# Kernel tuning notes

Hardware: AMD Instinct MI355X
Metric: run time of the kernel (lower is better)

The kernel has to match this reference:

```python
import jax, jax.numpy as jnp
import numpy as np

N = 8192
D_IN = 128
D_OUT = 64


def setup_inputs() -> dict:
    key = jax.random.key(0)
    k1, k2, k3 = jax.random.split(key, 3)
    features = jax.random.normal(k1, (N, D_IN), dtype=jnp.float32)
    # uniform [0,1) entries -> strictly positive row sums (degrees)
    adjacency_matrix = jax.random.uniform(k2, (N, N), dtype=jnp.float32)
    weight = jax.random.normal(k3, (D_IN, D_OUT), dtype=jnp.float32)
    return {"features": features, "adjacency_matrix": adjacency_matrix, "weight": weight}


def reference(features, adjacency_matrix, weight):
    # degree_matrix = diag(rowsum(A)); inverse(sqrt(diag(d))) == diag(d^{-1/2})
    deg = jnp.sum(adjacency_matrix, axis=1)            # [N]
    d_inv_sqrt = 1.0 / jnp.sqrt(deg)                   # [N]
    # D^{-1/2} A D^{-1/2} via broadcasting instead of dense diag matmuls
    norm_adj = d_inv_sqrt[:, None] * adjacency_matrix * d_inv_sqrt[None, :]  # [N,N]
    # (norm_adj @ X) @ W -- contract small dim last for efficiency
    h = norm_adj @ features                            # [N, D_IN]
    return jax.nn.relu(h @ weight)                     # [N, D_OUT]
```

## Files before the change

### kernel.cpp

```cpp
#include <hip/hip_runtime.h>

#define N_NODES 8192
#define D_IN    128
#define D_OUT   64
#define NSPLIT  16

typedef __attribute__((ext_vector_type(8))) short short8;
typedef __attribute__((ext_vector_type(4))) float f32x4;

__device__ __forceinline__ short f2bf(float f) {
    unsigned u = __builtin_bit_cast(unsigned, f);
    u += 0x7fff + ((u >> 16) & 1);
    return (short)(u >> 16);
}
__device__ __forceinline__ unsigned f2bf_pack(float lo, float hi) {
    unsigned a = __builtin_bit_cast(unsigned, lo);
    a += 0x7fff + ((a >> 16) & 1);
    unsigned b = __builtin_bit_cast(unsigned, hi);
    b += 0x7fff + ((b >> 16) & 1);
    return (a >> 16) | (b & 0xffff0000u);
}

__global__ __launch_bounds__(256) void k_deg(const float* __restrict__ A,
                                             float* __restrict__ dis,
                                             unsigned short* __restrict__ A16) {
    const int wave = threadIdx.x >> 6;
    const int lane = threadIdx.x & 63;
    const int row  = blockIdx.x * 4 + wave;
    const float4* Ar = (const float4*)(A + (size_t)row * N_NODES);
    uint2* Aw = (uint2*)(A16 + (size_t)row * N_NODES);
    float s = 0.f;
#pragma unroll
    for (int i = 0; i < 32; ++i) {
        float4 v = Ar[lane + 64 * i];
        s += (v.x + v.y) + (v.z + v.w);
        uint2 p;
        p.x = f2bf_pack(v.x, v.y);
        p.y = f2bf_pack(v.z, v.w);
        Aw[lane + 64 * i] = p;
    }
#pragma unroll
    for (int off = 32; off; off >>= 1) s += __shfl_down(s, off, 64);
    if (lane == 0) dis[row] = rsqrtf(s);
}

__global__ __launch_bounds__(256) void k_gpack(const float* __restrict__ X,
                                               const float* __restrict__ W,
                                               const float* __restrict__ dis,
                                               unsigned short* __restrict__ Gp) {
    __shared__ float Wl[D_IN * D_OUT];
    __shared__ float Xl[32 * 129];
    const int t = blockIdx.x, tid = threadIdx.x;

    const float4* W4 = (const float4*)W;
    float4* Wl4 = (float4*)Wl;
#pragma unroll
    for (int i = 0; i < 8; ++i) Wl4[tid + 256 * i] = W4[tid + 256 * i];
    const float4* X4 = (const float4*)(X + (size_t)t * 32 * D_IN);
#pragma unroll
    for (int i = 0; i < 4; ++i) {
        int idx = tid + 256 * i;
        float4 v = X4[idx];
        int r = idx >> 5, c = (idx & 31) * 4;
        float* dst = Xl + r * 129 + c;
        dst[0] = v.x; dst[1] = v.y; dst[2] = v.z; dst[3] = v.w;
    }
    __syncthreads();

    const int kl = tid & 31;
    const int nb = (tid >> 5) * 8;
    float acc[8] = {0.f,0.f,0.f,0.f,0.f,0.f,0.f,0.f};
    const float* xr = Xl + kl * 129;
    for (int d = 0; d < D_IN; ++d) {
        float xv = xr[d];
        const float* wr = Wl + d * D_OUT + nb;
#pragma unroll
        for (int c = 0; c < 8; ++c) acc[c] += xv * wr[c];
    }
    const float scale = dis[t * 32 + kl];
    const int quad = kl >> 3, j = kl & 7;
#pragma unroll
    for (int c = 0; c < 8; ++c) {
        int n = nb + c;
        int u = n >> 4;
        int lanei = quad * 16 + (n & 15);
        Gp[(((size_t)t * 4 + u) * 64 + lanei) * 8 + j] = (unsigned short)f2bf(acc[c] * scale);
    }
}

__global__ __launch_bounds__(256) void k_spmm(const unsigned short* __restrict__ A16,
                                              const unsigned short* __restrict__ Gp,
                                              float* __restrict__ partial) {
    const int lane = threadIdx.x & 63;
    const int wave = threadIdx.x >> 6;
    const int quad = lane >> 4;
    const int l15  = lane & 15;
    const int rowbase = blockIdx.x * 128 + wave * 32;

    const short8* Ar0 = (const short8*)(A16 + (size_t)(rowbase + l15) * N_NODES);
    const short8* Ar1 = (const short8*)(A16 + (size_t)(rowbase + 16 + l15) * N_NODES);
    const short8* Gq  = (const short8*)Gp;

    const int kt0 = blockIdx.y * (N_NODES / 32 / NSPLIT);
    f32x4 acc[2][4] = {};

    for (int kt = kt0; kt < kt0 + (N_NODES / 32 / NSPLIT); ++kt) {
        short8 a0 = Ar0[kt * 4 + quad];
        short8 a1 = Ar1[kt * 4 + quad];
        const short8* gb = Gq + (size_t)kt * 256 + lane;
#pragma unroll
        for (int u = 0; u < 4; ++u) {
            short8 b = gb[u * 64];
            acc[0][u] = __builtin_amdgcn_mfma_f32_16x16x32_bf16(a0, b, acc[0][u], 0, 0, 0);
            acc[1][u] = __builtin_amdgcn_mfma_f32_16x16x32_bf16(a1, b, acc[1][u], 0, 0, 0);
        }
    }

    float* P = partial + (size_t)blockIdx.y * (N_NODES * D_OUT);
#pragma unroll
    for (int rt = 0; rt < 2; ++rt)
#pragma unroll
        for (int u = 0; u < 4; ++u)
#pragma unroll
            for (int r = 0; r < 4; ++r) {
                int gr = rowbase + rt * 16 + quad * 4 + r;
                P[(size_t)gr * D_OUT + u * 16 + l15] = acc[rt][u][r];
            }
}

__global__ __launch_bounds__(256) void k_out(const float* __restrict__ partial,
                                             const float* __restrict__ dis,
                                             float* __restrict__ out) {
    const int idx = blockIdx.x * 256 + threadIdx.x;
    const float4* p4 = (const float4*)partial;
    float4 s = p4[idx];
#pragma unroll
    for (int sp = 1; sp < NSPLIT; ++sp) {
        float4 v = p4[idx + sp * (N_NODES * D_OUT / 4)];
        s.x += v.x; s.y += v.y; s.z += v.z; s.w += v.w;
    }
    const float sc = dis[idx >> 4];
    float4 o;
    o.x = fmaxf(s.x * sc, 0.f);
    o.y = fmaxf(s.y * sc, 0.f);
    o.z = fmaxf(s.z * sc, 0.f);
    o.w = fmaxf(s.w * sc, 0.f);
    ((float4*)out)[idx] = o;
}

extern "C" void kernel_launch(void* const* d_in, const int* in_sizes, int n_in,
                              void* d_out, int out_size, void* d_ws, size_t ws_size,
                              hipStream_t stream) {
    const float* X = (const float*)d_in[0];
    const float* A = (const float*)d_in[1];
    const float* W = (const float*)d_in[2];
    float* out = (float*)d_out;

    char* ws = (char*)d_ws;
    float*          dis     = (float*)ws;
    unsigned short* Gp      = (unsigned short*)(ws + (1u << 20));
    unsigned short* A16     = (unsigned short*)(ws + (2u << 20));
    float*          partial = (float*)(ws + (2u << 20) + ((size_t)128 << 20));

    k_deg  <<<N_NODES / 4, 256, 0, stream>>>(A, dis, A16);
    k_gpack<<<N_NODES / 32, 256, 0, stream>>>(X, W, dis, Gp);
    k_spmm <<<dim3(N_NODES / 128, NSPLIT), 256, 0, stream>>>(A16, Gp, partial);
    k_out  <<<(N_NODES * D_OUT / 4) / 256, 256, 0, stream>>>(partial, dis, out);
}
```

Before: 434.1 us.

## Fuse four kernels into one cooperative persistent kernel with grid syncs

Replaces the four separate launches (degree/convert, G pack, MFMA SpMM, split reduce) with one cooperative persistent kernel whose phases are separated by grid.sync, sized from occupancy and capped at 1024 blocks. The split-K factor is halved, which shrinks the partial buffer and the reduction work but leaves fewer parallel SpMM work items. The G-pack phase drops its LDS staging and reads W and X straight from global memory. This is meant to remove launch gaps and tail effects, at the cost of grid-sync overhead and possibly lower occupancy; if the cooperative launch fails, four kernels with fixed grids run instead.

```diff
diff --git a/kernel.cpp b/kernel.cpp
--- a/kernel.cpp
+++ b/kernel.cpp
@@ -1,9 +1,13 @@
 #include <hip/hip_runtime.h>
+#include <hip/hip_cooperative_groups.h>
+
+namespace cg = cooperative_groups;
 
 #define N_NODES 8192
 #define D_IN    128
 #define D_OUT   64
-#define NSPLIT  16
+#define NSPLIT  8
+#define MAXGRID 1024
 
 typedef __attribute__((ext_vector_type(8))) short short8;
 typedef __attribute__((ext_vector_type(4))) float f32x4;
@@ -21,131 +25,162 @@
     return (a >> 16) | (b & 0xffff0000u);
 }
 
-__global__ __launch_bounds__(256) void k_deg(const float* __restrict__ A,
-                                             float* __restrict__ dis,
-                                             unsigned short* __restrict__ A16) {
-    const int wave = threadIdx.x >> 6;
-    const int lane = threadIdx.x & 63;
-    const int row  = blockIdx.x * 4 + wave;
-    const float4* Ar = (const float4*)(A + (size_t)row * N_NODES);
-    uint2* Aw = (uint2*)(A16 + (size_t)row * N_NODES);
-    float s = 0.f;
-#pragma unroll
-    for (int i = 0; i < 32; ++i) {
-        float4 v = Ar[lane + 64 * i];
-        s += (v.x + v.y) + (v.z + v.w);
-        uint2 p;
-        p.x = f2bf_pack(v.x, v.y);
-        p.y = f2bf_pack(v.z, v.w);
-        Aw[lane + 64 * i] = p;
-    }
-#pragma unroll
-    for (int off = 32; off; off >>= 1) s += __shfl_down(s, off, 64);
-    if (lane == 0) dis[row] = rsqrtf(s);
-}
-
-__global__ __launch_bounds__(256) void k_gpack(const float* __restrict__ X,
-                                               const float* __restrict__ W,
-                                               const float* __restrict__ dis,
-                                               unsigned short* __restrict__ Gp) {
-    __shared__ float Wl[D_IN * D_OUT];
-    __shared__ float Xl[32 * 129];
-    const int t = blockIdx.x, tid = threadIdx.x;
-
-    const float4* W4 = (const float4*)W;
-    float4* Wl4 = (float4*)Wl;
-#pragma unroll
-    for (int i = 0; i < 8; ++i) Wl4[tid + 256 * i] = W4[tid + 256 * i];
-    const float4* X4 = (const float4*)(X + (size_t)t * 32 * D_IN);
-#pragma unroll
-    for (int i = 0; i < 4; ++i) {
-        int idx = tid + 256 * i;
-        float4 v = X4[idx];
-        int r = idx >> 5, c = (idx & 31) * 4;
-        float* dst = Xl + r * 129 + c;
-        dst[0] = v.x; dst[1] = v.y; dst[2] = v.z; dst[3] = v.w;
-    }
-    __syncthreads();
-
-    const int kl = tid & 31;
-    const int nb = (tid >> 5) * 8;
-    float acc[8] = {0.f,0.f,0.f,0.f,0.f,0.f,0.f,0.f};
-    const float* xr = Xl + kl * 129;
-    for (int d = 0; d < D_IN; ++d) {
-        float xv = xr[d];
-        const float* wr = Wl + d * D_OUT + nb;
-#pragma unroll
-        for (int c = 0; c < 8; ++c) acc[c] += xv * wr[c];
-    }
-    const float scale = dis[t * 32 + kl];
-    const int quad = kl >> 3, j = kl & 7;
-#pragma unroll
-    for (int c = 0; c < 8; ++c) {
-        int n = nb + c;
-        int u = n >> 4;
-        int lanei = quad * 16 + (n & 15);
-        Gp[(((size_t)t * 4 + u) * 64 + lanei) * 8 + j] = (unsigned short)f2bf(acc[c] * scale);
-    }
-}
-
-__global__ __launch_bounds__(256) void k_spmm(const unsigned short* __restrict__ A16,
-                                              const unsigned short* __restrict__ Gp,
-                                              float* __restrict__ partial) {
-    const int lane = threadIdx.x & 63;
-    const int wave = threadIdx.x >> 6;
-    const int quad = lane >> 4;
-    const int l15  = lane & 15;
-    const int rowbase = blockIdx.x * 128 + wave * 32;
-
-    const short8* Ar0 = (const short8*)(A16 + (size_t)(rowbase + l15) * N_NODES);
-    const short8* Ar1 = (const short8*)(A16 + (size_t)(rowbase + 16 + l15) * N_NODES);
-    const short8* Gq  = (const short8*)Gp;
-
-    const int kt0 = blockIdx.y * (N_NODES / 32 / NSPLIT);
-    f32x4 acc[2][4] = {};
-
-    for (int kt = kt0; kt < kt0 + (N_NODES / 32 / NSPLIT); ++kt) {
-        short8 a0 = Ar0[kt * 4 + quad];
-        short8 a1 = Ar1[kt * 4 + quad];
-        const short8* gb = Gq + (size_t)kt * 256 + lane;
-#pragma unroll
-        for (int u = 0; u < 4; ++u) {
-            short8 b = gb[u * 64];
-            acc[0][u] = __builtin_amdgcn_mfma_f32_16x16x32_bf16(a0, b, acc[0][u], 0, 0, 0);
-            acc[1][u] = __builtin_amdgcn_mfma_f32_16x16x32_bf16(a1, b, acc[1][u], 0, 0, 0);
-        }
-    }
-
-    float* P = partial + (size_t)blockIdx.y * (N_NODES * D_OUT);
-#pragma unroll
-    for (int rt = 0; rt < 2; ++rt)
-#pragma unroll
-        for (int u = 0; u < 4; ++u)
-#pragma unroll
-            for (int r = 0; r < 4; ++r) {
-                int gr = rowbase + rt * 16 + quad * 4 + r;
-                P[(size_t)gr * D_OUT + u * 16 + l15] = acc[rt][u][r];
+__device__ __forceinline__ void phase1(const float* __restrict__ A,
+                                       float* __restrict__ dis,
+                                       unsigned short* __restrict__ A16,
+                                       int bid, int nb, int tid) {
+    const int wave = tid >> 6, lane = tid & 63;
+    for (int row = bid * 4 + wave; row < N_NODES; row += nb * 4) {
+        const float4* Ar = (const float4*)(A + (size_t)row * N_NODES);
+        uint2* Aw = (uint2*)(A16 + (size_t)row * N_NODES);
+        float s = 0.f;
+#pragma unroll
+        for (int i = 0; i < 32; ++i) {
+            float4 v = Ar[lane + 64 * i];
+            s += (v.x + v.y) + (v.z + v.w);
+            uint2 p;
+            p.x = f2bf_pack(v.x, v.y);
+            p.y = f2bf_pack(v.z, v.w);
+            Aw[lane + 64 * i] = p;
+        }
+#pragma unroll
+        for (int off = 32; off; off >>= 1) s += __shfl_down(s, off, 64);
+        if (lane == 0) dis[row] = rsqrtf(s);
+    }
+}
+
+__device__ __forceinline__ void phase2(const float* __restrict__ X,
+                                       const float* __restrict__ W,
+                                       const float* __restrict__ dis,
+                                       unsigned short* __restrict__ Gp,
+                                       int bid, int nb, int tid) {
+    for (int gid = bid * 256 + tid; gid < N_NODES * 8; gid += nb * 256) {
+        const int k = gid >> 3;
+        const int n0 = (gid & 7) * 8;
+        float acc[8] = {0.f,0.f,0.f,0.f,0.f,0.f,0.f,0.f};
+        const float4* Xr = (const float4*)(X + (size_t)k * D_IN);
+#pragma unroll 4
+        for (int d4 = 0; d4 < 32; ++d4) {
+            float4 xv = Xr[d4];
+            const float* w = W + (d4 * 4) * D_OUT + n0;
+#pragma unroll
+            for (int q = 0; q < 4; ++q) {
+                float x = (q == 0) ? xv.x : (q == 1) ? xv.y : (q == 2) ? xv.z : xv.w;
+                float4 w0 = ((const float4*)(w + q * D_OUT))[0];
+                float4 w1 = ((const float4*)(w + q * D_OUT))[1];
+                acc[0] += x * w0.x; acc[1] += x * w0.y;
+                acc[2] += x * w0.z; acc[3] += x * w0.w;
+                acc[4] += x * w1.x; acc[5] += x * w1.y;
+                acc[6] += x * w1.z; acc[7] += x * w1.w;
             }
-}
-
-__global__ __launch_bounds__(256) void k_out(const float* __restrict__ partial,
-                                             const float* __restrict__ dis,
-                                             float* __restrict__ out) {
-    const int idx = blockIdx.x * 256 + threadIdx.x;
-    const float4* p4 = (const float4*)partial;
-    float4 s = p4[idx];
-#pragma unroll
-    for (int sp = 1; sp < NSPLIT; ++sp) {
-        float4 v = p4[idx + sp * (N_NODES * D_OUT / 4)];
-        s.x += v.x; s.y += v.y; s.z += v.z; s.w += v.w;
-    }
-    const float sc = dis[idx >> 4];
-    float4 o;
-    o.x = fmaxf(s.x * sc, 0.f);
-    o.y = fmaxf(s.y * sc, 0.f);
-    o.z = fmaxf(s.z * sc, 0.f);
-    o.w = fmaxf(s.w * sc, 0.f);
-    ((float4*)out)[idx] = o;
+        }
+        const float scale = dis[k];
+        const int t = k >> 5, quad = (k >> 3) & 3, j = k & 7;
+#pragma unroll
+        for (int c = 0; c < 8; ++c) {
+            int n = n0 + c;
+            Gp[(((size_t)t * 4 + (n >> 4)) * 64 + quad * 16 + (n & 15)) * 8 + j] =
+                (unsigned short)f2bf(acc[c] * scale);
+        }
+    }
+}
+
+__device__ __forceinline__ void phase3(const unsigned short* __restrict__ A16,
+                                       const unsigned short* __restrict__ Gp,
+                                       float* __restrict__ partial,
+                                       int bid, int nb, int tid) {
+    const int wave = tid >> 6, lane = tid & 63;
+    const int quad = lane >> 4, l15 = lane & 15;
+    const short8* Gq = (const short8*)Gp;
+    for (int w = bid; w < 64 * NSPLIT; w += nb) {
+        const int rowbase = (w & 63) * 128 + wave * 32;
+        const int split = w >> 6;
+        const short8* Ar0 = (const short8*)(A16 + (size_t)(rowbase + l15) * N_NODES);
+        const short8* Ar1 = (const short8*)(A16 + (size_t)(rowbase + 16 + l15) * N_NODES);
+        const int kt0 = split * (N_NODES / 32 / NSPLIT);
+        f32x4 acc[2][4] = {};
+        for (int kt = kt0; kt < kt0 + (N_NODES / 32 / NSPLIT); ++kt) {
+            short8 a0 = Ar0[kt * 4 + quad];
+            short8 a1 = Ar1[kt * 4 + quad];
+            const short8* gb = Gq + (size_t)kt * 256 + lane;
+#pragma unroll
+            for (int u = 0; u < 4; ++u) {
+                short8 b = gb[u * 64];
+                acc[0][u] = __builtin_amdgcn_mfma_f32_16x16x32_bf16(a0, b, acc[0][u], 0, 0, 0);
+                acc[1][u] = __builtin_amdgcn_mfma_f32_16x16x32_bf16(a1, b, acc[1][u], 0, 0, 0);
+            }
+        }
+        float* P = partial + (size_t)split * (N_NODES * D_OUT);
+#pragma unroll
+        for (int rt = 0; rt < 2; ++rt)
+#pragma unroll
+            for (int u = 0; u < 4; ++u)
+#pragma unroll
+                for (int r = 0; r < 4; ++r)
+                    P[(size_t)(rowbase + rt * 16 + quad * 4 + r) * D_OUT + u * 16 + l15] =
+                        acc[rt][u][r];
+    }
+}
+
+__device__ __forceinline__ void phase4(const float* __restrict__ partial,
+                                       const float* __restrict__ dis,
+                                       float* __restrict__ out,
+                                       int bid, int nb, int tid) {
+    for (int gid = bid * 256 + tid; gid < N_NODES * D_OUT / 4; gid += nb * 256) {
+        const float4* p4 = (const float4*)partial;
+        float4 s = p4[gid];
+#pragma unroll
+        for (int sp = 1; sp < NSPLIT; ++sp) {
+            float4 v = p4[gid + sp * (N_NODES * D_OUT / 4)];
+            s.x += v.x; s.y += v.y; s.z += v.z; s.w += v.w;
+        }
+        const float sc = dis[gid >> 4];
+        float4 o;
+        o.x = fmaxf(s.x * sc, 0.f);
+        o.y = fmaxf(s.y * sc, 0.f);
+        o.z = fmaxf(s.z * sc, 0.f);
+        o.w = fmaxf(s.w * sc, 0.f);
+        ((float4*)out)[gid] = o;
+    }
+}
+
+__global__ __launch_bounds__(256, 2) void k_fused(
+    const float* __restrict__ A, const float* __restrict__ X,
+    const float* __restrict__ W, float* __restrict__ dis,
+    unsigned short* __restrict__ A16, unsigned short* __restrict__ Gp,
+    float* __restrict__ partial, float* __restrict__ out)
+{
+    cg::grid_group grid = cg::this_grid();
+    const int bid = blockIdx.x, nb = gridDim.x, tid = threadIdx.x;
+    phase1(A, dis, A16, bid, nb, tid);
+    grid.sync();
+    phase2(X, W, dis, Gp, bid, nb, tid);
+    grid.sync();
+    phase3(A16, Gp, partial, bid, nb, tid);
+    grid.sync();
+    phase4(partial, dis, out, bid, nb, tid);
+}
+
+__global__ __launch_bounds__(256) void k_p1(const float* __restrict__ A,
+                                            float* __restrict__ dis,
+                                            unsigned short* __restrict__ A16) {
+    phase1(A, dis, A16, blockIdx.x, gridDim.x, threadIdx.x);
+}
+__global__ __launch_bounds__(256) void k_p2(const float* __restrict__ X,
+                                            const float* __restrict__ W,
+                                            const float* __restrict__ dis,
+                                            unsigned short* __restrict__ Gp) {
+    phase2(X, W, dis, Gp, blockIdx.x, gridDim.x, threadIdx.x);
+}
+__global__ __launch_bounds__(256) void k_p3(const unsigned short* __restrict__ A16,
+                                            const unsigned short* __restrict__ Gp,
+                                            float* __restrict__ partial) {
+    phase3(A16, Gp, partial, blockIdx.x, gridDim.x, threadIdx.x);
+}
+__global__ __launch_bounds__(256) void k_p4(const float* __restrict__ partial,
+                                            const float* __restrict__ dis,
+                                            float* __restrict__ out) {
+    phase4(partial, dis, out, blockIdx.x, gridDim.x, threadIdx.x);
 }
 
 extern "C" void kernel_launch(void* const* d_in, const int* in_sizes, int n_in,
@@ -162,8 +197,21 @@
     unsigned short* A16     = (unsigned short*)(ws + (2u << 20));
     float*          partial = (float*)(ws + (2u << 20) + ((size_t)128 << 20));
 
-    k_deg  <<<N_NODES / 4, 256, 0, stream>>>(A, dis, A16);
-    k_gpack<<<N_NODES / 32, 256, 0, stream>>>(X, W, dis, Gp);
-    k_spmm <<<dim3(N_NODES / 128, NSPLIT), 256, 0, stream>>>(A16, Gp, partial);
-    k_out  <<<(N_NODES * D_OUT / 4) / 256, 256, 0, stream>>>(partial, dis, out);
-}
+    int perCU = 0;
+    if (hipOccupancyMaxActiveBlocksPerMultiprocessor(&perCU, (const void*)k_fused,
+                                                     256, 0) != hipSuccess || perCU < 1)
+        perCU = 1;
+    int nblk = perCU * 256;
+    if (nblk > MAXGRID) nblk = MAXGRID;
+
+    void* args[] = { (void*)&A, (void*)&X, (void*)&W, (void*)&dis,
+                     (void*)&A16, (void*)&Gp, (void*)&partial, (void*)&out };
+    hipError_t err = hipLaunchCooperativeKernel((const void*)k_fused, dim3(nblk),
+                                                dim3(256), args, 0, stream);
+    if (err != hipSuccess) {
+        k_p1<<<2048, 256, 0, stream>>>(A, dis, A16);
+        k_p2<<<256, 256, 0, stream>>>(X, W, dis, Gp);
+        k_p3<<<512, 256, 0, stream>>>(A16, Gp, partial);
+        k_p4<<<512, 256, 0, stream>>>(partial, dis, out);
+    }
+}
```

Measured after the change: 621.3 us. 43.1% more time.

## Convert A to bf16 inside the matmul kernel instead of staging a bf16 copy

Applied to the files above, without the earlier changes.

Removes the bf16 copy of the adjacency matrix written by the degree kernel; the matmul kernel now reads fp32 A directly and converts it to bf16 in registers before the MFMAs. This eliminates a 128MB write and changes the memory traffic mix, at the cost of reading twice as many bytes of A in the matmul and extra conversion ALU work. It also doubles the K-split count (adding partial-sum traffic), rewrites the X·W kernel without shared memory, and batches loads in the degree kernel.

```diff
diff --git a/kernel.cpp b/kernel.cpp
--- a/kernel.cpp
+++ b/kernel.cpp
@@ -3,7 +3,7 @@
 #define N_NODES 8192
 #define D_IN    128
 #define D_OUT   64
-#define NSPLIT  16
+#define NSPLIT  32
 
 typedef __attribute__((ext_vector_type(8))) short short8;
 typedef __attribute__((ext_vector_type(4))) float f32x4;
@@ -13,31 +13,20 @@
     u += 0x7fff + ((u >> 16) & 1);
     return (short)(u >> 16);
 }
-__device__ __forceinline__ unsigned f2bf_pack(float lo, float hi) {
-    unsigned a = __builtin_bit_cast(unsigned, lo);
-    a += 0x7fff + ((a >> 16) & 1);
-    unsigned b = __builtin_bit_cast(unsigned, hi);
-    b += 0x7fff + ((b >> 16) & 1);
-    return (a >> 16) | (b & 0xffff0000u);
-}
 
 __global__ __launch_bounds__(256) void k_deg(const float* __restrict__ A,
-                                             float* __restrict__ dis,
-                                             unsigned short* __restrict__ A16) {
-    const int wave = threadIdx.x >> 6;
-    const int lane = threadIdx.x & 63;
-    const int row  = blockIdx.x * 4 + wave;
+                                             float* __restrict__ dis) {
+    const int wave = threadIdx.x >> 6, lane = threadIdx.x & 63;
+    const int row = blockIdx.x * 4 + wave;
     const float4* Ar = (const float4*)(A + (size_t)row * N_NODES);
-    uint2* Aw = (uint2*)(A16 + (size_t)row * N_NODES);
     float s = 0.f;
 #pragma unroll
-    for (int i = 0; i < 32; ++i) {
-        float4 v = Ar[lane + 64 * i];
-        s += (v.x + v.y) + (v.z + v.w);
-        uint2 p;
-        p.x = f2bf_pack(v.x, v.y);
-        p.y = f2bf_pack(v.z, v.w);
-        Aw[lane + 64 * i] = p;
+    for (int i = 0; i < 4; ++i) {
+        float4 v[8];
+#pragma unroll
+        for (int j = 0; j < 8; ++j) v[j] = Ar[lane + 64 * (i * 8 + j)];
+#pragma unroll
+        for (int j = 0; j < 8; ++j) s += (v[j].x + v[j].y) + (v[j].z + v[j].w);
     }
 #pragma unroll
     for (int off = 32; off; off >>= 1) s += __shfl_down(s, off, 64);
@@ -48,104 +37,100 @@
                                                const float* __restrict__ W,
                                                const float* __restrict__ dis,
                                                unsigned short* __restrict__ Gp) {
-    __shared__ float Wl[D_IN * D_OUT];
-    __shared__ float Xl[32 * 129];
-    const int t = blockIdx.x, tid = threadIdx.x;
-
-    const float4* W4 = (const float4*)W;
-    float4* Wl4 = (float4*)Wl;
+    const int gid = blockIdx.x * 256 + threadIdx.x;
+    if (gid >= N_NODES * 8) return;
+    const int k = gid >> 3;
+    const int n0 = (gid & 7) * 8;
+    float acc[8] = {0.f,0.f,0.f,0.f,0.f,0.f,0.f,0.f};
+    const float4* Xr = (const float4*)(X + (size_t)k * D_IN);
+#pragma unroll 4
+    for (int d4 = 0; d4 < 32; ++d4) {
+        float4 xv = Xr[d4];
+        const float* w = W + (d4 * 4) * D_OUT + n0;
 #pragma unroll
-    for (int i = 0; i < 8; ++i) Wl4[tid + 256 * i] = W4[tid + 256 * i];
-    const float4* X4 = (const float4*)(X + (size_t)t * 32 * D_IN);
-#pragma unroll
-    for (int i = 0; i < 4; ++i) {
-        int idx = tid + 256 * i;
-        float4 v = X4[idx];
-        int r = idx >> 5, c = (idx & 31) * 4;
-        float* dst = Xl + r * 129 + c;
-        dst[0] = v.x; dst[1] = v.y; dst[2] = v.z; dst[3] = v.w;
+        for (int q = 0; q < 4; ++q) {
+            float x = (q == 0) ? xv.x : (q == 1) ? xv.y : (q == 2) ? xv.z : xv.w;
+            float4 w0 = ((const float4*)(w + q * D_OUT))[0];
+            float4 w1 = ((const float4*)(w + q * D_OUT))[1];
+            acc[0] += x * w0.x; acc[1] += x * w0.y;
+            acc[2] += x * w0.z; acc[3] += x * w0.w;
+            acc[4] += x * w1.x; acc[5] += x * w1.y;
+            acc[6] += x * w1.z; acc[7] += x * w1.w;
+        }
     }
-    __syncthreads();
-
-    const int kl = tid & 31;
-    const int nb = (tid >> 5) * 8;
-    float acc[8] = {0.f,0.f,0.f,0.f,0.f,0.f,0.f,0.f};
-    const float* xr = Xl + kl * 129;
-    for (int d = 0; d < D_IN; ++d) {
-        float xv = xr[d];
-        const float* wr = Wl + d * D_OUT + nb;
-#pragma unroll
-        for (int c = 0; c < 8; ++c) acc[c] += xv * wr[c];
-    }
-    const float scale = dis[t * 32 + kl];
-    const int quad = kl >> 3, j = kl & 7;
+    const float scale = dis[k];
+    const int t = k >> 5, quad = (k >> 3) & 3, j = k & 7;
 #pragma unroll
     for (int c = 0; c < 8; ++c) {
-        int n = nb + c;
-        int u = n >> 4;
-        int lanei = quad * 16 + (n & 15);
-        Gp[(((size_t)t * 4 + u) * 64 + lanei) * 8 + j] = (unsigned short)f2bf(acc[c] * scale);
+        int n = n0 + c;
+        Gp[(((size_t)t * 4 + (n >> 4)) * 64 + quad * 16 + (n & 15)) * 8 + j] =
+            (unsigned short)f2bf(acc[c] * scale);
     }
 }
 
-__global__ __launch_bounds__(256) void k_spmm(const unsigned short* __restrict__ A16,
-                                              const unsigned short* __restrict__ Gp,
-                                              float* __restrict__ partial) {
-    const int lane = threadIdx.x & 63;
-    const int wave = threadIdx.x >> 6;
-    const int quad = lane >> 4;
-    const int l15  = lane & 15;
+__global__ __launch_bounds__(256, 4) void k_spmm(const float* __restrict__ A,
+                                                 const unsigned short* __restrict__ Gp,
+                                                 float* __restrict__ partial) {
+    const int lane = threadIdx.x & 63, wave = threadIdx.x >> 6;
+    const int quad = lane >> 4, l15 = lane & 15;
     const int rowbase = blockIdx.x * 128 + wave * 32;
-
-    const short8* Ar0 = (const short8*)(A16 + (size_t)(rowbase + l15) * N_NODES);
-    const short8* Ar1 = (const short8*)(A16 + (size_t)(rowbase + 16 + l15) * N_NODES);
-    const short8* Gq  = (const short8*)Gp;
-
+    const float* Ar0 = A + (size_t)(rowbase + l15) * N_NODES;
+    const float* Ar1 = A + (size_t)(rowbase + 16 + l15) * N_NODES;
+    const short8* Gq = (const short8*)Gp;
     const int kt0 = blockIdx.y * (N_NODES / 32 / NSPLIT);
     f32x4 acc[2][4] = {};
-
+#pragma unroll 2
     for (int kt = kt0; kt < kt0 + (N_NODES / 32 / NSPLIT); ++kt) {
-        short8 a0 = Ar0[kt * 4 + quad];
-        short8 a1 = Ar1[kt * 4 + quad];
+        const int col = kt * 32 + quad * 8;
+        float4 a0lo = *(const float4*)(Ar0 + col);
+        float4 a0hi = *(const float4*)(Ar0 + col + 4);
+        float4 a1lo = *(const float4*)(Ar1 + col);
+        float4 a1hi = *(const float4*)(Ar1 + col + 4);
         const short8* gb = Gq + (size_t)kt * 256 + lane;
-#pragma unroll
-        for (int u = 0; u < 4; ++u) {
-            short8 b = gb[u * 64];
-            acc[0][u] = __builtin_amdgcn_mfma_f32_16x16x32_bf16(a0, b, acc[0][u], 0, 0, 0);
-            acc[1][u] = __builtin_amdgcn_mfma_f32_16x16x32_bf16(a1, b, acc[1][u], 0, 0, 0);
-        }
+        short8 b0 = gb[0], b1 = gb[64], b2 = gb[128], b3 = gb[192];
+        short8 a0, a1;
+        a0[0]=f2bf(a0lo.x); a0[1]=f2bf(a0lo.y); a0[2]=f2bf(a0lo.z); a0[3]=f2bf(a0lo.w);
+        a0[4]=f2bf(a0hi.x); a0[5]=f2bf(a0hi.y); a0[6]=f2bf(a0hi.z); a0[7]=f2bf(a0hi.w);
+        a1[0]=f2bf(a1lo.x); a1[1]=f2bf(a1lo.y); a1[2]=f2bf(a1lo.z); a1[3]=f2bf(a1lo.w);
+        a1[4]=f2bf(a1hi.x); a1[5]=f2bf(a1hi.y); a1[6]=f2bf(a1hi.z); a1[7]=f2bf(a1hi.w);
+        acc[0][0] = __builtin_amdgcn_mfma_f32_16x16x32_bf16(a0, b0, acc[0][0], 0, 0, 0);
+        acc[1][0] = __builtin_amdgcn_mfma_f32_16x16x32_bf16(a1, b0, acc[1][0], 0, 0, 0);
+        acc[0][1] = __builtin_amdgcn_mfma_f32_16x16x32_bf16(a0, b1, acc[0][1], 0, 0, 0);
+        acc[1][1] = __builtin_amdgcn_mfma_f32_16x16x32_bf16(a1, b1, acc[1][1], 0, 0, 0);
+        acc[0][2] = __builtin_amdgcn_mfma_f32_16x16x32_bf16(a0, b2, acc[0][2], 0, 0, 0);
+        acc[1][2] = __builtin_amdgcn_mfma_f32_16x16x32_bf16(a1, b2, acc[1][2], 0, 0, 0);
+        acc[0][3] = __builtin_amdgcn_mfma_f32_16x16x32_bf16(a0, b3, acc[0][3], 0, 0, 0);
+        acc[1][3] = __builtin_amdgcn_mfma_f32_16x16x32_bf16(a1, b3, acc[1][3], 0, 0, 0);
     }
-
     float* P = partial + (size_t)blockIdx.y * (N_NODES * D_OUT);
 #pragma unroll
     for (int rt = 0; rt < 2; ++rt)
 #pragma unroll
         for (int u = 0; u < 4; ++u)
 #pragma unroll
-            for (int r = 0; r < 4; ++r) {
-                int gr = rowbase + rt * 16 + quad * 4 + r;
-                P[(size_t)gr * D_OUT + u * 16 + l15] = acc[rt][u][r];
-            }
+            for (int r = 0; r < 4; ++r)
+                P[(size_t)(rowbase + rt * 16 + quad * 4 + r) * D_OUT + u * 16 + l15] =
+                    acc[rt][u][r];
 }
 
 __global__ __launch_bounds__(256) void k_out(const float* __restrict__ partial,
                                              const float* __restrict__ dis,
                                              float* __restrict__ out) {
-    const int idx = blockIdx.x * 256 + threadIdx.x;
+    const int gid = blockIdx.x * 256 + threadIdx.x;
     const float4* p4 = (const float4*)partial;
-    float4 s = p4[idx];
+    float4 s = p4[gid];
 #pragma unroll
     for (int sp = 1; sp < NSPLIT; ++sp) {
-        float4 v = p4[idx + sp * (N_NODES * D_OUT / 4)];
+        float4 v = p4[gid + (size_t)sp * (N_NODES * D_OUT / 4)];
         s.x += v.x; s.y += v.y; s.z += v.z; s.w += v.w;
     }
-    const float sc = dis[idx >> 4];
+    const float sc = dis[gid >> 4];
     float4 o;
     o.x = fmaxf(s.x * sc, 0.f);
     o.y = fmaxf(s.y * sc, 0.f);
     o.z = fmaxf(s.z * sc, 0.f);
     o.w = fmaxf(s.w * sc, 0.f);
-    ((float4*)out)[idx] = o;
+    ((float4*)out)[gid] = o;
 }
 
 extern "C" void kernel_launch(void* const* d_in, const int* in_sizes, int n_in,
@@ -159,11 +144,10 @@
     char* ws = (char*)d_ws;
     float*          dis     = (float*)ws;
     unsigned short* Gp      = (unsigned short*)(ws + (1u << 20));
-    unsigned short* A16     = (unsigned short*)(ws + (2u << 20));
-    float*          partial = (float*)(ws + (2u << 20) + ((size_t)128 << 20));
+    float*          partial = (float*)(ws + (4u << 20));
 
-    k_deg  <<<N_NODES / 4, 256, 0, stream>>>(A, dis, A16);
-    k_gpack<<<N_NODES / 32, 256, 0, stream>>>(X, W, dis, Gp);
-    k_spmm <<<dim3(N_NODES / 128, NSPLIT), 256, 0, stream>>>(A16, Gp, partial);
+    k_deg  <<<N_NODES / 4, 256, 0, stream>>>(A, dis);
+    k_gpack<<<N_NODES * 8 / 256, 256, 0, stream>>>(X, W, dis, Gp);
+    k_spmm <<<dim3(N_NODES / 128, NSPLIT), 256, 0, stream>>>(A, Gp, partial);
     k_out  <<<(N_NODES * D_OUT / 4) / 256, 256, 0, stream>>>(partial, dis, out);
 }
```

Measured after the change: 461.7 us. 1.06x slower.
